# Kernel tuning notes

Hardware: AMD Instinct MI355X
Metric: run time of the kernel (lower is better)

Reference implementation:

```python
import jax, jax.numpy as jnp
import numpy as np

N = 50000   # nodes
E = 800000  # edges (avg degree 16)
D = 128     # in_dim == hidden_dim


def setup_inputs() -> dict:
    key = jax.random.key(0)
    ks = jax.random.split(key, 8)
    x = jax.random.normal(ks[0], (N, D), dtype=jnp.float32)
    edge_index = jax.random.randint(ks[1], (2, E), 0, N, dtype=jnp.int32)
    s = 1.0 / np.sqrt(D)  # glorot-ish scale
    W0 = jax.random.normal(ks[2], (D, D), dtype=jnp.float32) * s
    W1 = jax.random.normal(ks[3], (D, D), dtype=jnp.float32) * s
    W2 = jax.random.normal(ks[4], (D, D), dtype=jnp.float32) * s
    b0 = jnp.zeros((D,), dtype=jnp.float32)
    b1 = jnp.zeros((D,), dtype=jnp.float32)
    b2 = jnp.zeros((D,), dtype=jnp.float32)
    return {"x": x, "edge_index": edge_index,
            "W0": W0, "b0": b0, "W1": W1, "b1": b1, "W2": W2, "b2": b2}


def reference(x, edge_index, W0, b0, W1, b1, W2, b2):
    # PyG GCNConv defaults: add self-loops, symmetric D^-1/2 (A+I) D^-1/2 norm,
    # linear transform first, bias added after aggregation.
    src, dst = edge_index[0], edge_index[1]
    loops = jnp.arange(N, dtype=src.dtype)
    src_f = jnp.concatenate([src, loops])  # [E+N]
    dst_f = jnp.concatenate([dst, loops])
    deg = jax.ops.segment_sum(jnp.ones_like(src_f, dtype=x.dtype), dst_f, num_segments=N)
    dinv = jnp.where(deg > 0, jax.lax.rsqrt(deg), 0.0)
    norm = dinv[src_f] * dinv[dst_f]  # [E+N]

    def gcn_layer(h, W, b):
        h = h @ W                                # [N, D]
        msg = h[src_f] * norm[:, None]           # [E+N, D] gather
        agg = jax.ops.segment_sum(msg, dst_f, num_segments=N)  # scatter-add
        return agg + b

    h = jax.nn.relu(gcn_layer(x, W0, b0))  # dropout p=0.0 is a no-op
    h = jax.nn.relu(gcn_layer(h, W1, b1))
    return gcn_layer(h, W2, b2)
```

## Files before the change

kernel.cpp:

```cpp
#include <hip/hip_runtime.h>
#include <hip/hip_fp16.h>

#define NN 50000
#define NPAD 50048
#define NE 800000
#define D 128
#define BPAD 136
#define EGRID 3125
#define NB 196
#define GGRID 782
#define DSLICE 6250

typedef __attribute__((ext_vector_type(8))) short bf16x8;
typedef __attribute__((ext_vector_type(4))) float f32x4;

__device__ inline unsigned short f2bf(float f) {
    unsigned int b = __float_as_uint(f);
    return (unsigned short)((b + 0x7FFFu + ((b >> 16) & 1u)) >> 16);
}
__device__ inline float bf2f(unsigned short u) {
    return __uint_as_float(((unsigned int)u) << 16);
}


__global__ void k_degree_convW(const int* __restrict__ dst, int* __restrict__ cnt,
                               int* __restrict__ rank, int* __restrict__ counter,
                               const float* __restrict__ W0, const float* __restrict__ W1,
                               const float* __restrict__ W2,
                               unsigned short* __restrict__ Wh, unsigned short* __restrict__ Wl) {
    int bid = blockIdx.x;
    int t = threadIdx.x;
    if (bid == 0 && t == 0) counter[0] = 0;
    if (bid < EGRID) {
        int e = bid * 256 + t;
        if (e < NE) {
            int d = dst[e];
            int r = atomicAdd(&cnt[d], 1);
            __builtin_nontemporal_store(r, &rank[e]);
        }
    } else {
        int i = (bid - EGRID) * 256 + t;
        if (i >= 3 * D * D) return;
        int m = i / (D * D), r = i - m * (D * D);
        const float* W = (m == 0) ? W0 : ((m == 1) ? W1 : W2);
        int k = r >> 7, c = r & 127;
        float v = W[r];
        unsigned short h = f2bf(v);
        unsigned short l = f2bf(v - bf2f(h));
        Wh[(size_t)m * D * D + c * D + k] = h;
        Wl[(size_t)m * D * D + c * D + k] = l;
    }
}

__global__ void k_scan_block(const int* __restrict__ cnt, int* __restrict__ excl,
                             int* __restrict__ bsum, int* __restrict__ boff,
                             int* __restrict__ counter) {
    __shared__ int sm[256];
    __shared__ int lastflag;
    int t = threadIdx.x;
    int idx = blockIdx.x * 256 + t;
    int v = (idx < NN) ? cnt[idx] : 0;
    sm[t] = v;
    __syncthreads();
    for (int o = 1; o < 256; o <<= 1) {
        int u = (t >= o) ? sm[t - o] : 0;
        __syncthreads();
        sm[t] += u;
        __syncthreads();
    }
    if (idx < NN) excl[idx] = sm[t] - v;
    if (t == 255) bsum[blockIdx.x] = sm[255];
    __threadfence();
    if (t == 0) {
        int ticket = atomicAdd(counter, 1);
        lastflag = (ticket == NB - 1);
    }
    __syncthreads();
    if (!lastflag) return;
    __threadfence();
    int v2 = (t < NB) ? bsum[t] : 0;
    sm[t] = v2;
    __syncthreads();
    for (int o = 1; o < 256; o <<= 1) {
        int u = (t >= o) ? sm[t - o] : 0;
        __syncthreads();
        sm[t] += u;
        __syncthreads();
    }
    if (t < NB) boff[t] = sm[t] - v2;
}

__global__ void k_scan_add(int* __restrict__ rowptr, const int* __restrict__ boff,
                           const int* __restrict__ cnt, float* __restrict__ dinv) {
    int idx = blockIdx.x * 256 + threadIdx.x;
    if (idx < NN) {
        rowptr[idx] += boff[idx >> 8];
        dinv[idx] = rsqrtf((float)(cnt[idx] + 1));
    } else if (idx == NN) {
        rowptr[NN] = NE;
    }
}


__device__ inline void gemm_store(f32x4 acc[2][4], const float* __restrict__ dinv,
                                  __half* __restrict__ C, int R0, int C0, int lr, int lg) {
    #pragma unroll
    for (int fr = 0; fr < 2; fr++) {
        int rb = R0 + fr * 16 + lg * 4;
        #pragma unroll
        for (int j = 0; j < 4; j++) {
            int r = rb + j;
            if (r < NN) {
                float s = dinv[r];
                #pragma unroll
                for (int fc = 0; fc < 4; fc++)
                    C[(size_t)r * D + C0 + fc * 16 + lr] =
                        __float2half_rn(acc[fr][fc][j] * s);
            }
        }
    }
}


__global__ __launch_bounds__(256, 2) void k_fill_gemm_x(
        const int* __restrict__ src, const int* __restrict__ dst,
        const int* __restrict__ rowptr, const int* __restrict__ rank,
        int* __restrict__ col,
        const float* __restrict__ X,
        const unsigned short* __restrict__ BhT, const unsigned short* __restrict__ BlT,
        const float* __restrict__ dinv, __half* __restrict__ C) {
    __shared__ short Bs_h[D * BPAD];
    int t = threadIdx.x;
    if (blockIdx.x >= GGRID) {
        int slice = blockIdx.x & 7;
        int chunk = (blockIdx.x - GGRID) >> 3;
        int e = chunk * 256 + t;
        if (e < NE) {
            int d = dst[e];
            if (d / DSLICE == slice) {
                int pos = rowptr[d] + rank[e];
                __builtin_nontemporal_store(src[e], &col[pos]);
            }
        }
        return;
    }
    {
        int c = t >> 1;
        int k0 = (t & 1) * 64;
        const unsigned short* gh = BhT + c * D + k0;
        short* dh = Bs_h + c * BPAD + k0;
        #pragma unroll
        for (int i = 0; i < 8; i++)
            *(int4*)(dh + i * 8) = *(const int4*)(gh + i * 8);
    }
    __syncthreads();

    int w = t >> 6, ln = t & 63;
    int wr = w >> 1, wc = w & 1;
    int R0 = blockIdx.x * 64 + wr * 32;
    int C0 = wc * 64;
    int lr = ln & 15, lg = ln >> 4;

    f32x4 acc[2][4];
    #pragma unroll
    for (int a = 0; a < 2; a++)
        #pragma unroll
        for (int b = 0; b < 4; b++)
            acc[a][b] = (f32x4){0.f, 0.f, 0.f, 0.f};

    const float* Ab = X + (size_t)(R0 + lr) * D + lg * 8;

    #pragma unroll
    for (int ks = 0; ks < 4; ks++) {
        int ko = ks * 32;
        bf16x8 fa_h[2], fa_l[2], fb_h[4], fb_l[4];
        #pragma unroll
        for (int fr = 0; fr < 2; fr++) {
            float4 p0 = *(const float4*)(Ab + fr * 16 * D + ko);
            float4 p1 = *(const float4*)(Ab + fr * 16 * D + ko + 4);
            float vv[8] = {p0.x, p0.y, p0.z, p0.w, p1.x, p1.y, p1.z, p1.w};
            #pragma unroll
            for (int j = 0; j < 8; j++) {
                unsigned short h = f2bf(vv[j]);
                fa_h[fr][j] = (short)h;
                fa_l[fr][j] = (short)f2bf(vv[j] - bf2f(h));
            }
        }
        #pragma unroll
        for (int fc = 0; fc < 4; fc++) {
            int ccol = C0 + fc * 16 + lr;
            fb_h[fc] = *(const bf16x8*)(Bs_h + ccol * BPAD + ko + lg * 8);
            fb_l[fc] = *(const bf16x8*)(BlT + (size_t)ccol * D + ko + lg * 8);
        }
        #pragma unroll
        for (int fr = 0; fr < 2; fr++) {
            #pragma unroll
            for (int fc = 0; fc < 4; fc++) {
                acc[fr][fc] = __builtin_amdgcn_mfma_f32_16x16x32_bf16(
                    fa_h[fr], fb_h[fc], acc[fr][fc], 0, 0, 0);
                acc[fr][fc] = __builtin_amdgcn_mfma_f32_16x16x32_bf16(
                    fa_l[fr], fb_h[fc], acc[fr][fc], 0, 0, 0);
                acc[fr][fc] = __builtin_amdgcn_mfma_f32_16x16x32_bf16(
                    fa_h[fr], fb_l[fc], acc[fr][fc], 0, 0, 0);
            }
        }
    }
    gemm_store(acc, dinv, C, R0, C0, lr, lg);
}


__global__ __launch_bounds__(256, 3) void k_gemm_mfma_h(
        const __half* __restrict__ H,
        const unsigned short* __restrict__ BhT, const unsigned short* __restrict__ BlT,
        const float* __restrict__ dinv, __half* __restrict__ C) {
    __shared__ short Bs_h[D * BPAD];
    int t = threadIdx.x;
    {
        int c = t >> 1;
        int k0 = (t & 1) * 64;
        const unsigned short* gh = BhT + c * D + k0;
        short* dh = Bs_h + c * BPAD + k0;
        #pragma unroll
        for (int i = 0; i < 8; i++)
            *(int4*)(dh + i * 8) = *(const int4*)(gh + i * 8);
    }
    __syncthreads();

    int w = t >> 6, ln = t & 63;
    int wr = w >> 1, wc = w & 1;
    int R0 = blockIdx.x * 64 + wr * 32;
    int C0 = wc * 64;
    int lr = ln & 15, lg = ln >> 4;

    f32x4 acc[2][4];
    #pragma unroll
    for (int a = 0; a < 2; a++)
        #pragma unroll
        for (int b = 0; b < 4; b++)
            acc[a][b] = (f32x4){0.f, 0.f, 0.f, 0.f};

    const __half* Ab = H + (size_t)(R0 + lr) * D + lg * 8;

    #pragma unroll
    for (int ks = 0; ks < 4; ks++) {
        int ko = ks * 32;
        bf16x8 fa_h[2], fa_l[2], fb_h[4], fb_l[4];
        #pragma unroll
        for (int fr = 0; fr < 2; fr++) {
            float4 p = *(const float4*)(Ab + fr * 16 * D + ko);
            const __half2* hp = (const __half2*)&p;
            #pragma unroll
            for (int q = 0; q < 4; q++) {
                float2 fv = __half22float2(hp[q]);
                unsigned short h0 = f2bf(fv.x), h1 = f2bf(fv.y);
                fa_h[fr][q * 2]     = (short)h0;
                fa_h[fr][q * 2 + 1] = (short)h1;
                fa_l[fr][q * 2]     = (short)f2bf(fv.x - bf2f(h0));
                fa_l[fr][q * 2 + 1] = (short)f2bf(fv.y - bf2f(h1));
            }
        }
        #pragma unroll
        for (int fc = 0; fc < 4; fc++) {
            int ccol = C0 + fc * 16 + lr;
            fb_h[fc] = *(const bf16x8*)(Bs_h + ccol * BPAD + ko + lg * 8);
            fb_l[fc] = *(const bf16x8*)(BlT + (size_t)ccol * D + ko + lg * 8);
        }
        #pragma unroll
        for (int fr = 0; fr < 2; fr++) {
            #pragma unroll
            for (int fc = 0; fc < 4; fc++) {
                acc[fr][fc] = __builtin_amdgcn_mfma_f32_16x16x32_bf16(
                    fa_h[fr], fb_h[fc], acc[fr][fc], 0, 0, 0);
                acc[fr][fc] = __builtin_amdgcn_mfma_f32_16x16x32_bf16(
                    fa_l[fr], fb_h[fc], acc[fr][fc], 0, 0, 0);
                acc[fr][fc] = __builtin_amdgcn_mfma_f32_16x16x32_bf16(
                    fa_h[fr], fb_l[fc], acc[fr][fc], 0, 0, 0);
            }
        }
    }
    gemm_store(acc, dinv, C, R0, C0, lr, lg);
}


__device__ inline void agg_accum(const float4& rv, float a[8]) {
    const __half2* hp = (const __half2*)&rv;
    #pragma unroll
    for (int q = 0; q < 4; q++) {
        float2 fv = __half22float2(hp[q]);
        a[q * 2] += fv.x;
        a[q * 2 + 1] += fv.y;
    }
}

__device__ inline void agg_core(const __half* __restrict__ T,
                                const int* __restrict__ rowptr,
                                const int* __restrict__ col,
                                int i, int f, int lane, float a[8]) {
    int gb = lane & 48;
    int sl16 = lane & 15;
    {
        float4 raw = *(const float4*)(T + (size_t)i * D + f);
        const __half2* hp = (const __half2*)&raw;
        #pragma unroll
        for (int q = 0; q < 4; q++) {
            float2 fv = __half22float2(hp[q]);
            a[q * 2] = fv.x;
            a[q * 2 + 1] = fv.y;
        }
    }
    int r0 = rowptr[i], r1 = rowptr[i + 1];
    for (int e = r0; e < r1; e += 16) {
        int idx = e + sl16;
        if (idx > r1 - 1) idx = r1 - 1;
        int cv = col[idx];
        int m = r1 - e;
        m = m > 16 ? 16 : m;
        int ss[16];
        #pragma unroll
        for (int u = 0; u < 16; u++) ss[u] = __shfl(cv, gb + u, 64);
        float4 rv[16];
        #pragma unroll
        for (int u = 0; u < 16; u++)
            rv[u] = *(const float4*)(T + (size_t)ss[u] * D + f);
        #pragma unroll
        for (int u = 0; u < 16; u++)
            if (u < m) agg_accum(rv[u], a);
    }
}

__global__ __launch_bounds__(256) void k_agg_relu(const __half* __restrict__ T,
                                                  const int* __restrict__ rowptr,
                                                  const int* __restrict__ col,
                                                  const float* __restrict__ dinv,
                                                  const float* __restrict__ bias,
                                                  __half* __restrict__ Hout) {
    int i = blockIdx.x * 16 + (threadIdx.x >> 4);
    int lane = threadIdx.x & 63;
    int sl = threadIdx.x & 15;
    int f = sl * 8;
    float di = dinv[i];
    float a[8];
    agg_core(T, rowptr, col, i, f, lane, a);
    float4 bv0 = *(const float4*)(bias + f);
    float4 bv1 = *(const float4*)(bias + f + 4);
    float bb[8] = {bv0.x, bv0.y, bv0.z, bv0.w, bv1.x, bv1.y, bv1.z, bv1.w};
    __half2 o[4];
    #pragma unroll
    for (int q = 0; q < 4; q++) {
        float x0 = fmaxf(a[q * 2] * di + bb[q * 2], 0.f);
        float x1 = fmaxf(a[q * 2 + 1] * di + bb[q * 2 + 1], 0.f);
        o[q] = __floats2half2_rn(x0, x1);
    }
    *(float4*)(Hout + (size_t)i * D + f) = *(float4*)o;
}

__global__ __launch_bounds__(256) void k_agg_out(const __half* __restrict__ T,
                                                 const int* __restrict__ rowptr,
                                                 const int* __restrict__ col,
                                                 const float* __restrict__ dinv,
                                                 const float* __restrict__ bias,
                                                 float* __restrict__ Of) {
    int i = blockIdx.x * 16 + (threadIdx.x >> 4);
    int lane = threadIdx.x & 63;
    int sl = threadIdx.x & 15;
    int f = sl * 8;
    float di = dinv[i];
    float a[8];
    agg_core(T, rowptr, col, i, f, lane, a);
    float4 bv0 = *(const float4*)(bias + f);
    float4 bv1 = *(const float4*)(bias + f + 4);
    float4 o0 = make_float4(a[0] * di + bv0.x, a[1] * di + bv0.y,
                            a[2] * di + bv0.z, a[3] * di + bv0.w);
    float4 o1 = make_float4(a[4] * di + bv1.x, a[5] * di + bv1.y,
                            a[6] * di + bv1.z, a[7] * di + bv1.w);
    *(float4*)(Of + (size_t)i * D + f) = o0;
    *(float4*)(Of + (size_t)i * D + f + 4) = o1;
}


extern "C" void kernel_launch(void* const* d_in, const int* in_sizes, int n_in,
                              void* d_out, int out_size, void* d_ws, size_t ws_size,
                              hipStream_t stream) {
    const float* x  = (const float*)d_in[0];
    const int* edge = (const int*)d_in[1];
    const float* W0 = (const float*)d_in[2];
    const float* b0 = (const float*)d_in[3];
    const float* W1 = (const float*)d_in[4];
    const float* b1 = (const float*)d_in[5];
    const float* W2 = (const float*)d_in[6];
    const float* b2 = (const float*)d_in[7];
    const int* src = edge;
    const int* dst = edge + NE;
    float* out = (float*)d_out;

    char* ws = (char*)d_ws;
    size_t off = 0;
    auto alloc = [&](size_t bytes) {
        void* p = ws + off;
        off += (bytes + 255) & ~(size_t)255;
        return p;
    };
    int*   cnt     = (int*)alloc(NN * 4);
    int*   counter = (int*)alloc(256);
    int*   rowptr  = (int*)alloc((NN + 1) * 4);
    float* dinv    = (float*)alloc(NN * 4);
    int*   bsum    = (int*)alloc(256 * 4);
    int*   boff    = (int*)alloc(256 * 4);
    int*   rank    = (int*)alloc((size_t)NE * 4);
    int*   col     = (int*)alloc((size_t)NE * 4);
    unsigned short* Wh = (unsigned short*)alloc(3 * D * D * 2);
    unsigned short* Wl = (unsigned short*)alloc(3 * D * D * 2);
    __half* Ta = (__half*)alloc((size_t)NPAD * D * 2);
    __half* Tb = (__half*)alloc((size_t)NPAD * D * 2);
    __half* Hb = (__half*)alloc((size_t)NPAD * D * 2);

    hipMemsetAsync(cnt, 0, NN * 4, stream);

    k_degree_convW<<<EGRID + 192, 256, 0, stream>>>(dst, cnt, rank, counter,
                                                    W0, W1, W2, Wh, Wl);
    k_scan_block<<<NB, 256, 0, stream>>>(cnt, rowptr, bsum, boff, counter);
    k_scan_add<<<(NN + 256) / 256, 256, 0, stream>>>(rowptr, boff, cnt, dinv);

    const int agrid = NN / 16;

    k_fill_gemm_x<<<GGRID + 8 * EGRID, 256, 0, stream>>>(src, dst, rowptr, rank, col,
                                                         x, Wh, Wl, dinv, Ta);
    k_agg_relu<<<agrid, 256, 0, stream>>>(Ta, rowptr, col, dinv, b0, Hb);
    k_gemm_mfma_h<<<GGRID, 256, 0, stream>>>(Hb, Wh + D * D, Wl + D * D, dinv, Tb);
    k_agg_relu<<<agrid, 256, 0, stream>>>(Tb, rowptr, col, dinv, b1, Hb);
    k_gemm_mfma_h<<<GGRID, 256, 0, stream>>>(Hb, Wh + 2 * D * D, Wl + 2 * D * D, dinv, Ta);
    k_agg_out<<<agrid, 256, 0, stream>>>(Ta, rowptr, col, dinv, b2, out);
}
```

Measured before the change: 249.7 us.

## Drop scan-add kernel, compute row offsets and dinv on the fly

Removes the k_scan_add launch. Consumers now compute row offsets as excl[i]+boff[i>>8] and the normalisation as rsqrt(cnt+1) inline. The col fill no longer uses 8 dst-sliced passes and instead does a single pass over edges, which cuts the fill grid from 8x to 1x EGRID but spreads the scattered writes more widely. The MFMA GEMM launch bound also rises to 4 blocks per SM. The price is some extra loads and rsqrt work in each consumer.

```diff
diff --git a/kernel.cpp b/kernel.cpp
--- a/kernel.cpp
+++ b/kernel.cpp
@@ -9,7 +9,6 @@
 #define EGRID 3125
 #define NB 196
 #define GGRID 782
-#define DSLICE 6250
 
 typedef __attribute__((ext_vector_type(8))) short bf16x8;
 typedef __attribute__((ext_vector_type(4))) float f32x4;
@@ -90,19 +89,8 @@
     if (t < NB) boff[t] = sm[t] - v2;
 }
 
-__global__ void k_scan_add(int* __restrict__ rowptr, const int* __restrict__ boff,
-                           const int* __restrict__ cnt, float* __restrict__ dinv) {
-    int idx = blockIdx.x * 256 + threadIdx.x;
-    if (idx < NN) {
-        rowptr[idx] += boff[idx >> 8];
-        dinv[idx] = rsqrtf((float)(cnt[idx] + 1));
-    } else if (idx == NN) {
-        rowptr[NN] = NE;
-    }
-}
-
-
-__device__ inline void gemm_store(f32x4 acc[2][4], const float* __restrict__ dinv,
+
+__device__ inline void gemm_store(f32x4 acc[2][4], const int* __restrict__ cnt,
                                   __half* __restrict__ C, int R0, int C0, int lr, int lg) {
     #pragma unroll
     for (int fr = 0; fr < 2; fr++) {
@@ -111,7 +99,7 @@
         for (int j = 0; j < 4; j++) {
             int r = rb + j;
             if (r < NN) {
-                float s = dinv[r];
+                float s = rsqrtf((float)(cnt[r] + 1));
                 #pragma unroll
                 for (int fc = 0; fc < 4; fc++)
                     C[(size_t)r * D + C0 + fc * 16 + lr] =
@@ -124,23 +112,19 @@
 
 __global__ __launch_bounds__(256, 2) void k_fill_gemm_x(
         const int* __restrict__ src, const int* __restrict__ dst,
-        const int* __restrict__ rowptr, const int* __restrict__ rank,
-        int* __restrict__ col,
+        const int* __restrict__ excl, const int* __restrict__ boff,
+        const int* __restrict__ rank, int* __restrict__ col,
         const float* __restrict__ X,
         const unsigned short* __restrict__ BhT, const unsigned short* __restrict__ BlT,
-        const float* __restrict__ dinv, __half* __restrict__ C) {
+        const int* __restrict__ cnt, __half* __restrict__ C) {
     __shared__ short Bs_h[D * BPAD];
     int t = threadIdx.x;
     if (blockIdx.x >= GGRID) {
-        int slice = blockIdx.x & 7;
-        int chunk = (blockIdx.x - GGRID) >> 3;
-        int e = chunk * 256 + t;
+        int e = (blockIdx.x - GGRID) * 256 + t;
         if (e < NE) {
             int d = dst[e];
-            if (d / DSLICE == slice) {
-                int pos = rowptr[d] + rank[e];
-                __builtin_nontemporal_store(src[e], &col[pos]);
-            }
+            int pos = excl[d] + boff[d >> 8] + rank[e];
+            __builtin_nontemporal_store(src[e], &col[pos]);
         }
         return;
     }
@@ -205,14 +189,14 @@
             }
         }
     }
-    gemm_store(acc, dinv, C, R0, C0, lr, lg);
-}
-
-
-__global__ __launch_bounds__(256, 3) void k_gemm_mfma_h(
+    gemm_store(acc, cnt, C, R0, C0, lr, lg);
+}
+
+
+__global__ __launch_bounds__(256, 4) void k_gemm_mfma_h(
         const __half* __restrict__ H,
         const unsigned short* __restrict__ BhT, const unsigned short* __restrict__ BlT,
-        const float* __restrict__ dinv, __half* __restrict__ C) {
+        const int* __restrict__ cnt, __half* __restrict__ C) {
     __shared__ short Bs_h[D * BPAD];
     int t = threadIdx.x;
     {
@@ -278,7 +262,7 @@
             }
         }
     }
-    gemm_store(acc, dinv, C, R0, C0, lr, lg);
+    gemm_store(acc, cnt, C, R0, C0, lr, lg);
 }
 
 
@@ -293,7 +277,8 @@
 }
 
 __device__ inline void agg_core(const __half* __restrict__ T,
-                                const int* __restrict__ rowptr,
+                                const int* __restrict__ excl,
+                                const int* __restrict__ boff,
                                 const int* __restrict__ col,
                                 int i, int f, int lane, float a[8]) {
     int gb = lane & 48;
@@ -308,7 +293,8 @@
             a[q * 2 + 1] = fv.y;
         }
     }
-    int r0 = rowptr[i], r1 = rowptr[i + 1];
+    int r0 = excl[i] + boff[i >> 8];
+    int r1 = (i == NN - 1) ? NE : (excl[i + 1] + boff[(i + 1) >> 8]);
     for (int e = r0; e < r1; e += 16) {
         int idx = e + sl16;
         if (idx > r1 - 1) idx = r1 - 1;
@@ -329,18 +315,19 @@
 }
 
 __global__ __launch_bounds__(256) void k_agg_relu(const __half* __restrict__ T,
-                                                  const int* __restrict__ rowptr,
+                                                  const int* __restrict__ excl,
+                                                  const int* __restrict__ boff,
                                                   const int* __restrict__ col,
-                                                  const float* __restrict__ dinv,
+                                                  const int* __restrict__ cnt,
                                                   const float* __restrict__ bias,
                                                   __half* __restrict__ Hout) {
     int i = blockIdx.x * 16 + (threadIdx.x >> 4);
     int lane = threadIdx.x & 63;
     int sl = threadIdx.x & 15;
     int f = sl * 8;
-    float di = dinv[i];
+    float di = rsqrtf((float)(cnt[i] + 1));
     float a[8];
-    agg_core(T, rowptr, col, i, f, lane, a);
+    agg_core(T, excl, boff, col, i, f, lane, a);
     float4 bv0 = *(const float4*)(bias + f);
     float4 bv1 = *(const float4*)(bias + f + 4);
     float bb[8] = {bv0.x, bv0.y, bv0.z, bv0.w, bv1.x, bv1.y, bv1.z, bv1.w};
@@ -355,18 +342,19 @@
 }
 
 __global__ __launch_bounds__(256) void k_agg_out(const __half* __restrict__ T,
-                                                 const int* __restrict__ rowptr,
+                                                 const int* __restrict__ excl,
+                                                 const int* __restrict__ boff,
                                                  const int* __restrict__ col,
-                                                 const float* __restrict__ dinv,
+                                                 const int* __restrict__ cnt,
                                                  const float* __restrict__ bias,
                                                  float* __restrict__ Of) {
     int i = blockIdx.x * 16 + (threadIdx.x >> 4);
     int lane = threadIdx.x & 63;
     int sl = threadIdx.x & 15;
     int f = sl * 8;
-    float di = dinv[i];
+    float di = rsqrtf((float)(cnt[i] + 1));
     float a[8];
-    agg_core(T, rowptr, col, i, f, lane, a);
+    agg_core(T, excl, boff, col, i, f, lane, a);
     float4 bv0 = *(const float4*)(bias + f);
     float4 bv1 = *(const float4*)(bias + f + 4);
     float4 o0 = make_float4(a[0] * di + bv0.x, a[1] * di + bv0.y,
@@ -402,8 +390,7 @@
     };
     int*   cnt     = (int*)alloc(NN * 4);
     int*   counter = (int*)alloc(256);
-    int*   rowptr  = (int*)alloc((NN + 1) * 4);
-    float* dinv    = (float*)alloc(NN * 4);
+    int*   excl    = (int*)alloc(NN * 4);
     int*   bsum    = (int*)alloc(256 * 4);
     int*   boff    = (int*)alloc(256 * 4);
     int*   rank    = (int*)alloc((size_t)NE * 4);
@@ -418,16 +405,15 @@
 
     k_degree_convW<<<EGRID + 192, 256, 0, stream>>>(dst, cnt, rank, counter,
                                                     W0, W1, W2, Wh, Wl);
-    k_scan_block<<<NB, 256, 0, stream>>>(cnt, rowptr, bsum, boff, counter);
-    k_scan_add<<<(NN + 256) / 256, 256, 0, stream>>>(rowptr, boff, cnt, dinv);
+    k_scan_block<<<NB, 256, 0, stream>>>(cnt, excl, bsum, boff, counter);
 
     const int agrid = NN / 16;
 
-    k_fill_gemm_x<<<GGRID + 8 * EGRID, 256, 0, stream>>>(src, dst, rowptr, rank, col,
-                                                         x, Wh, Wl, dinv, Ta);
-    k_agg_relu<<<agrid, 256, 0, stream>>>(Ta, rowptr, col, dinv, b0, Hb);
-    k_gemm_mfma_h<<<GGRID, 256, 0, stream>>>(Hb, Wh + D * D, Wl + D * D, dinv, Tb);
-    k_agg_relu<<<agrid, 256, 0, stream>>>(Tb, rowptr, col, dinv, b1, Hb);
-    k_gemm_mfma_h<<<GGRID, 256, 0, stream>>>(Hb, Wh + 2 * D * D, Wl + 2 * D * D, dinv, Ta);
-    k_agg_out<<<agrid, 256, 0, stream>>>(Ta, rowptr, col, dinv, b2, out);
-}
+    k_fill_gemm_x<<<GGRID + EGRID, 256, 0, stream>>>(src, dst, excl, boff, rank, col,
+                                                     x, Wh, Wl, cnt, Ta);
+    k_agg_relu<<<agrid, 256, 0, stream>>>(Ta, excl, boff, col, cnt, b0, Hb);
+    k_gemm_mfma_h<<<GGRID, 256, 0, stream>>>(Hb, Wh + D * D, Wl + D * D, cnt, Tb);
+    k_agg_relu<<<agrid, 256, 0, stream>>>(Tb, excl, boff, col, cnt, b1, Hb);
+    k_gemm_mfma_h<<<GGRID, 256, 0, stream>>>(Hb, Wh + 2 * D * D, Wl + 2 * D * D, cnt, Ta);
+    k_agg_out<<<agrid, 256, 0, stream>>>(Ta, excl, boff, col, cnt, b2, out);
+}
```

Measured after the change: 230.8 us. 1.08x faster.
